# Optimization experiments

Measured on AMD Instinct MI355X. Metric: run time of the kernel, lower is better.

The kernel has to match this reference:

```python
import jax, jax.numpy as jnp
import numpy as np

B, S, D, H, DK = 2, 2048, 256, 8, 32


def setup_inputs() -> dict:
    key = jax.random.key(0)
    ks = jax.random.split(key, 12)
    inp = {
        "query": jax.random.normal(ks[0], (B, S, D), jnp.float32),
        "key_": jax.random.normal(ks[1], (B, S, D), jnp.float32),
        "value": jax.random.normal(ks[2], (B, S, D), jnp.float32),
        "mask": jax.random.randint(ks[3], (B, S, S), 0, 2).astype(bool),
        "relation": jax.random.normal(ks[4], (B, S, S), jnp.float32) * 0.05,
        # learned params (Linear stores y = x @ W^T; we store W already transposed)
        "Wq": jax.random.normal(ks[5], (D, H * DK), jnp.float32) * 0.02,
        "Wk": jax.random.normal(ks[6], (D, H * DK), jnp.float32) * 0.02,
        "Wv": jax.random.normal(ks[7], (D, H * DK), jnp.float32) * 0.02,
        "Wfc": jax.random.normal(ks[8], (H * DK, D), jnp.float32) * 0.02,
        "bfc": jax.random.normal(ks[9], (D,), jnp.float32) * 0.02,
        "gamma": jnp.ones((D,), jnp.float32),
        "beta": jnp.zeros((D,), jnp.float32),
    }
    return inp


def _layernorm(x, gamma, beta, eps=1e-5):
    mu = jnp.mean(x, axis=-1, keepdims=True)
    var = jnp.var(x, axis=-1, keepdims=True)
    return (x - mu) * jax.lax.rsqrt(var + eps) * gamma + beta


def reference(query, key_, value, mask, relation, Wq, Wk, Wv, Wfc, bfc, gamma, beta):
    b, s, _ = query.shape
    def split_heads(x, W):
        return (x @ W).reshape(b, s, H, DK).transpose(0, 2, 1, 3)  # [B,H,S,DK]
    Q = split_heads(query, Wq)
    K = split_heads(key_, Wk)
    V = split_heads(value, Wv)
    # (Q K^T) @ relation / sqrt(dk)   -- relation broadcast over heads
    qk = jnp.einsum('bhqd,bhkd->bhqk', Q, K)          # [B,H,S,S]
    scores = jnp.einsum('bhqk,bkn->bhqn', qk, relation) / jnp.sqrt(jnp.float32(DK))
    scores = jnp.where(mask[:, None, :, :], jnp.float32(-1e9), scores)
    attn = jax.nn.softmax(scores, axis=-1)            # dropout in eval mode = identity
    att = jnp.einsum('bhqn,bhnd->bhqd', attn, V)      # [B,H,S,DK]
    att = att.transpose(0, 2, 1, 3).reshape(b, s, H * DK)
    out = att @ Wfc + bfc
    return _layernorm(out + query, gamma, beta), attn
```

## Files before the change

kernel.cpp:

```cpp
#include <hip/hip_runtime.h>

constexpr int Bc = 2, Sc = 2048, Dc = 256, Hc = 8, DKc = 32;
constexpr int BH = Bc * Hc;

typedef _Float16 f16x8 __attribute__((ext_vector_type(8)));
typedef _Float16 f16x4 __attribute__((ext_vector_type(4)));
typedef float    f32x4 __attribute__((ext_vector_type(4)));

__global__ __launch_bounds__(256) void prep_kernel(
    const float* __restrict__ query, const float* __restrict__ key_,
    const float* __restrict__ value, const float* __restrict__ Wq,
    const float* __restrict__ Wk, const float* __restrict__ Wv,
    const float* __restrict__ rel, const unsigned int* __restrict__ mask,
    _Float16* __restrict__ Qb, _Float16* __restrict__ Kt,
    _Float16* __restrict__ Vt, _Float16* __restrict__ relT,
    unsigned int* __restrict__ mbits)
{
    __shared__ __align__(16) char smem[16640];
    const int bx = blockIdx.x;
    const int t = threadIdx.x;
    if (bx < 1536) {
        constexpr int ROWS = 8;
        float (*xs)[Dc] = (float(*)[Dc])smem;
        const int z = bx >> 9;
        const int lb = bx & 511;
        const float* X = (z == 0) ? query : (z == 1) ? key_ : value;
        const float* W = (z == 0) ? Wq : (z == 1) ? Wk : Wv;
        _Float16* out = (z == 0) ? Qb : (z == 1) ? Kt : Vt;
        const int vtrans = (z != 0);
        const float scale = (z == 0) ? 0.17677669529663689f : 1.0f;
        const int r0 = lb * ROWS;
        #pragma unroll
        for (int i = 0; i < ROWS; ++i)
            xs[i][t] = X[(long)(r0 + i) * Dc + t];
        __syncthreads();
        float acc[ROWS];
        #pragma unroll
        for (int i = 0; i < ROWS; ++i) acc[i] = 0.f;
        for (int d = 0; d < Dc; ++d) {
            float w = W[d * Dc + t];
            #pragma unroll
            for (int i = 0; i < ROWS; ++i) acc[i] = fmaf(xs[i][d], w, acc[i]);
        }
        const int h = t >> 5, dk = t & 31;
        #pragma unroll
        for (int i = 0; i < ROWS; ++i) {
            int row = r0 + i;
            int b = row >> 11, s = row & 2047;
            long idx = vtrans ? (((long)(b * Hc + h) * DKc + dk) * Sc + s)
                              : (((long)(b * Hc + h) * Sc + s) * DKc + dk);
            out[idx] = (_Float16)(acc[i] * scale);
        }
    } else if (bx < 3584) {
        float (*tile)[65] = (float(*)[65])smem;
        const int idx = bx - 1536;
        const int b = idx >> 10;
        const int rem = idx & 1023;
        const int k0 = (rem >> 5) * 64, n0 = (rem & 31) * 64;
        const int r = t >> 4;
        const int c4 = (t & 15) * 4;
        const float* src = rel + (long)b * Sc * Sc;
        #pragma unroll
        for (int i = 0; i < 4; ++i) {
            f32x4 v = *(const f32x4*)&src[(long)(k0 + i * 16 + r) * Sc + n0 + c4];
            *(f32x4*)&tile[i * 16 + r][c4] = v;
        }
        __syncthreads();
        _Float16* dst = relT + (long)b * Sc * Sc;
        #pragma unroll
        for (int i = 0; i < 4; ++i) {
            const int n = i * 16 + r;
            f16x4 o;
            #pragma unroll
            for (int e = 0; e < 4; ++e) o[e] = (_Float16)tile[c4 + e][n];
            *(f16x4*)&dst[(long)(n0 + n) * Sc + k0 + c4] = o;
        }
    } else {
        const int idx = (bx - 3584) * 256 + t;
        const uint4 a = ((const uint4*)mask)[idx * 2];
        const uint4 b = ((const uint4*)mask)[idx * 2 + 1];
        unsigned int wsv[8] = {a.x, a.y, a.z, a.w, b.x, b.y, b.z, b.w};
        unsigned int r = 0;
        #pragma unroll
        for (int j = 0; j < 8; ++j) {
            unsigned int nib = (wsv[j] | (wsv[j] >> 7) | (wsv[j] >> 14) | (wsv[j] >> 21)) & 0xFu;
            r |= nib << (4 * j);
        }
        mbits[idx] = r;
    }
}

__global__ __launch_bounds__(256) void kr_kernel(
    const _Float16* __restrict__ relT, const _Float16* __restrict__ Kt,
    float* __restrict__ KRp)
{
    constexpr int LDK = 72;
    __shared__ _Float16 As[64][LDK];
    __shared__ _Float16 Bs[64][LDK];
    const int z = blockIdx.z;
    const int b = z >> 1, ks = z & 1;
    const int m0 = blockIdx.y * 64;
    const int n0 = blockIdx.x * 64;
    const _Float16* Ap = relT + (long)b * Sc * Sc;
    const _Float16* Bp = Kt + (long)b * Hc * DKc * Sc;
    const int t = threadIdx.x;
    const int lane = t & 63, wave = t >> 6;
    const int wr = wave >> 1, wc = wave & 1;
    const int c = lane & 15, g = lane >> 4;
    const int lrow = t >> 2;
    const int lcol = (t & 3) * 16;
    f32x4 acc[2][2] = {};
    for (int k0 = ks * 1024; k0 < ks * 1024 + 1024; k0 += 64) {
        *(f16x8*)&As[lrow][lcol]     = *(const f16x8*)&Ap[(long)(m0 + lrow) * Sc + k0 + lcol];
        *(f16x8*)&As[lrow][lcol + 8] = *(const f16x8*)&Ap[(long)(m0 + lrow) * Sc + k0 + lcol + 8];
        *(f16x8*)&Bs[lrow][lcol]     = *(const f16x8*)&Bp[(long)(n0 + lrow) * Sc + k0 + lcol];
        *(f16x8*)&Bs[lrow][lcol + 8] = *(const f16x8*)&Bp[(long)(n0 + lrow) * Sc + k0 + lcol + 8];
        __syncthreads();
        #pragma unroll
        for (int kk = 0; kk < 2; ++kk) {
            const int kb = kk * 32 + g * 8;
            f16x8 af[2], bf[2];
            #pragma unroll
            for (int m = 0; m < 2; ++m)
                af[m] = *(const f16x8*)&As[wr * 32 + m * 16 + c][kb];
            #pragma unroll
            for (int n = 0; n < 2; ++n)
                bf[n] = *(const f16x8*)&Bs[wc * 32 + n * 16 + c][kb];
            #pragma unroll
            for (int m = 0; m < 2; ++m)
                #pragma unroll
                for (int n = 0; n < 2; ++n)
                    acc[m][n] = __builtin_amdgcn_mfma_f32_16x16x32_f16(
                        af[m], bf[n], acc[m][n], 0, 0, 0);
        }
        __syncthreads();
    }
    float* outp = KRp + ((long)ks * Bc + b) * Sc * 256;
    #pragma unroll
    for (int m = 0; m < 2; ++m)
        #pragma unroll
        for (int n = 0; n < 2; ++n)
            #pragma unroll
            for (int i = 0; i < 4; ++i) {
                int row = m0 + wr * 32 + m * 16 + g * 4 + i;
                int col = n0 + wc * 32 + n * 16 + c;
                outp[(long)row * 256 + col] = acc[m][n][i];
            }
}

__global__ __launch_bounds__(256) void krc_kernel(
    const float* __restrict__ KRp, _Float16* __restrict__ KRT)
{
    const long idx = ((long)blockIdx.x * 256 + threadIdx.x) * 4;
    const long half = (long)Bc * Sc * 256;
    f32x4 a = *(const f32x4*)&KRp[idx];
    f32x4 b = *(const f32x4*)&KRp[half + idx];
    f16x4 o;
    #pragma unroll
    for (int i = 0; i < 4; ++i) o[i] = (_Float16)(a[i] + b[i]);
    *(f16x4*)&KRT[idx] = o;
}

__global__ __launch_bounds__(256) void attn_pv_kernel(
    const _Float16* __restrict__ Qb,
    const _Float16* __restrict__ KRT,
    const _Float16* __restrict__ Vt,
    const unsigned int* __restrict__ mbits,
    float* __restrict__ esum_p,
    float* __restrict__ accp)
{
    constexpr int NT = 128, LDP = 136;
    __shared__ _Float16 p_lds[64][LDP];
    const int bh = blockIdx.y;
    const int ns = blockIdx.z;
    const int b = bh >> 3, h = bh & 7;
    const int q0 = blockIdx.x * 64;
    const int t = threadIdx.x, lane = t & 63, w = t >> 6;
    const int c = lane & 15, g = lane >> 4;
    const int q = q0 + w * 16 + c;
    const f16x8 qf = *(const f16x8*)&Qb[((long)bh * Sc + q) * DKc + g * 8];
    const _Float16* krt = KRT + (long)b * Sc * 256 + h * 32;
    const unsigned int* mbitrow = mbits + ((long)b * Sc + q) * (Sc / 32);
    const f32x4 zero = {};
    f32x4 acc[2] = {};
    float esum = 0.f;

    for (int nt = ns * 4; nt < ns * 4 + 4; ++nt) {
        const int n0 = nt * NT;
        f32x4 s[8];
        #pragma unroll
        for (int nf = 0; nf < 8; ++nf) {
            f16x8 kf = *(const f16x8*)&krt[(long)(n0 + nf * 16 + c) * 256 + g * 8];
            s[nf] = __builtin_amdgcn_mfma_f32_16x16x32_f16(kf, qf, zero, 0, 0, 0);
        }
        const uint4 mq = *(const uint4*)&mbitrow[nt * 4];
        const unsigned int mwv[4] = {mq.x, mq.y, mq.z, mq.w};
        #pragma unroll
        for (int nf = 0; nf < 8; ++nf) {
            const unsigned int bits = mwv[nf >> 1] >> ((nf & 1) * 16 + g * 4);
            f16x4 pv;
            #pragma unroll
            for (int i = 0; i < 4; ++i) {
                float p = ((bits >> i) & 1u) ? 0.f : __expf(s[nf][i]);
                esum += p;
                pv[i] = (_Float16)p;
            }
            *(f16x4*)&p_lds[w * 16 + c][nf * 16 + g * 4] = pv;
        }
        #pragma unroll
        for (int ks = 0; ks < 4; ++ks) {
            f16x8 af = *(const f16x8*)&p_lds[w * 16 + c][ks * 32 + g * 8];
            #pragma unroll
            for (int nb = 0; nb < 2; ++nb) {
                f16x8 vf = *(const f16x8*)&Vt[((long)bh * DKc + nb * 16 + c) * Sc + n0 + ks * 32 + g * 8];
                acc[nb] = __builtin_amdgcn_mfma_f32_16x16x32_f16(af, vf, acc[nb], 0, 0, 0);
            }
        }
    }
    esum += __shfl_xor(esum, 16);
    esum += __shfl_xor(esum, 32);
    if (lane < 16)
        esum_p[((long)ns * BH + bh) * Sc + q0 + w * 16 + lane] = esum;
    #pragma unroll
    for (int nb = 0; nb < 2; ++nb)
        #pragma unroll
        for (int i = 0; i < 4; ++i) {
            const long qrow = q0 + w * 16 + g * 4 + i;
            accp[(((long)ns * BH + bh) * Sc + qrow) * 32 + nb * 16 + c] = acc[nb][i];
        }
}

__global__ __launch_bounds__(256) void attn_store_kernel(
    const _Float16* __restrict__ Qb,
    const _Float16* __restrict__ KRT,
    const unsigned int* __restrict__ mbits,
    const float* __restrict__ esum_p,
    float* __restrict__ attn_out)
{
    constexpr int LDA = 132;
    __shared__ float a_lds[4][16][LDA];
    const int nt = blockIdx.x;
    const int q0 = blockIdx.y * 64;
    const int bh = blockIdx.z;
    const int b = bh >> 3, h = bh & 7;
    const int t = threadIdx.x, lane = t & 63, w = t >> 6;
    const int c = lane & 15, g = lane >> 4;
    const int q = q0 + w * 16 + c;
    const int n0 = nt * 128;
    const f16x8 qf = *(const f16x8*)&Qb[((long)bh * Sc + q) * DKc + g * 8];
    const _Float16* krt = KRT + (long)b * Sc * 256 + h * 32;
    const long row = (long)bh * Sc + q;
    const long BHS = (long)BH * Sc;
    const float es = esum_p[row] + esum_p[BHS + row]
                   + esum_p[2 * BHS + row] + esum_p[3 * BHS + row];
    const float rinv = 1.f / es;
    const f32x4 zero = {};

    f32x4 s[8];
    #pragma unroll
    for (int nf = 0; nf < 8; ++nf) {
        f16x8 kf = *(const f16x8*)&krt[(long)(n0 + nf * 16 + c) * 256 + g * 8];
        s[nf] = __builtin_amdgcn_mfma_f32_16x16x32_f16(kf, qf, zero, 0, 0, 0);
    }
    const uint4 mq = *(const uint4*)&mbits[((long)b * Sc + q) * (Sc / 32) + nt * 4];
    const unsigned int mwv[4] = {mq.x, mq.y, mq.z, mq.w};
    #pragma unroll
    for (int nf = 0; nf < 8; ++nf) {
        const unsigned int bits = mwv[nf >> 1] >> ((nf & 1) * 16 + g * 4);
        f32x4 av;
        #pragma unroll
        for (int i = 0; i < 4; ++i)
            av[i] = ((bits >> i) & 1u) ? 0.f : __expf(s[nf][i]) * rinv;
        *(f32x4*)&a_lds[w][c][nf * 16 + g * 4] = av;
    }
    float* aoutw = attn_out + (long)bh * Sc * Sc
                 + (long)(q0 + w * 16 + (lane >> 5)) * Sc + (lane & 31) * 4 + n0;
    #pragma unroll
    for (int r2 = 0; r2 < 8; ++r2) {
        f32x4 v = *(const f32x4*)&a_lds[w][r2 * 2 + (lane >> 5)][(lane & 31) * 4];
        __builtin_nontemporal_store(v, (f32x4*)&aoutw[(long)(r2 * 2) * Sc]);
    }
}

__global__ __launch_bounds__(256) void out_kernel(
    const float* __restrict__ accp,
    const float* __restrict__ esum_p,
    const float* __restrict__ Wfc,
    const float* __restrict__ bfc, const float* __restrict__ query,
    const float* __restrict__ gamma, const float* __restrict__ beta,
    float* __restrict__ out)
{
    __shared__ float xs[4][Dc];
    __shared__ float ys[4][Dc];
    const int r0 = blockIdx.x * 4;
    const int t = threadIdx.x;
    const int h = t >> 5, dk = t & 31;
    const long BHS = (long)BH * Sc;
    #pragma unroll
    for (int i = 0; i < 4; ++i) {
        const long row = r0 + i;
        const int b = (int)(row >> 11);
        const int q = (int)(row & 2047);
        const long bhq = ((long)(b * Hc + h)) * Sc + q;
        float es = 0.f, av = 0.f;
        #pragma unroll
        for (int ns = 0; ns < 4; ++ns) {
            es += esum_p[ns * BHS + bhq];
            av += accp[(ns * BHS + bhq) * 32 + dk];
        }
        xs[i][t] = av / es;
    }
    __syncthreads();
    float acc[4] = {0.f, 0.f, 0.f, 0.f};
    for (int d = 0; d < Dc; ++d) {
        float wv = Wfc[d * Dc + t];
        #pragma unroll
        for (int i = 0; i < 4; ++i) acc[i] = fmaf(xs[i][d], wv, acc[i]);
    }
    const float bias = bfc[t];
    #pragma unroll
    for (int i = 0; i < 4; ++i)
        ys[i][t] = acc[i] + bias + query[(long)(r0 + i) * Dc + t];
    __syncthreads();
    const int w = t >> 6, lane = t & 63;
    float x0 = ys[w][lane], x1 = ys[w][lane + 64];
    float x2 = ys[w][lane + 128], x3 = ys[w][lane + 192];
    float sum = x0 + x1 + x2 + x3;
    float sq = x0 * x0 + x1 * x1 + x2 * x2 + x3 * x3;
    for (int off = 32; off; off >>= 1) {
        sum += __shfl_down(sum, off);
        sq  += __shfl_down(sq, off);
    }
    sum = __shfl(sum, 0);
    sq  = __shfl(sq, 0);
    const float mu = sum * (1.f / 256.f);
    const float var = sq * (1.f / 256.f) - mu * mu;
    const float rstd = rsqrtf(var + 1e-5f);
    float* orow = out + (long)(r0 + w) * Dc;
    orow[lane]       = (x0 - mu) * rstd * gamma[lane]       + beta[lane];
    orow[lane + 64]  = (x1 - mu) * rstd * gamma[lane + 64]  + beta[lane + 64];
    orow[lane + 128] = (x2 - mu) * rstd * gamma[lane + 128] + beta[lane + 128];
    orow[lane + 192] = (x3 - mu) * rstd * gamma[lane + 192] + beta[lane + 192];
}

extern "C" void kernel_launch(void* const* d_in, const int* in_sizes, int n_in,
                              void* d_out, int out_size, void* d_ws, size_t ws_size,
                              hipStream_t stream)
{
    const float* query   = (const float*)d_in[0];
    const float* key_    = (const float*)d_in[1];
    const float* value   = (const float*)d_in[2];
    const unsigned int* mask = (const unsigned int*)d_in[3];
    const float* relation = (const float*)d_in[4];
    const float* Wq  = (const float*)d_in[5];
    const float* Wk  = (const float*)d_in[6];
    const float* Wv  = (const float*)d_in[7];
    const float* Wfc = (const float*)d_in[8];
    const float* bfc = (const float*)d_in[9];
    const float* gamma = (const float*)d_in[10];
    const float* beta  = (const float*)d_in[11];

    float* out_ln   = (float*)d_out;
    float* out_attn = (float*)d_out + (size_t)Bc * Sc * Dc;

    char* ws = (char*)d_ws;
    _Float16* Qb   = (_Float16*)(ws + 0);
    _Float16* Kt   = (_Float16*)(ws + 2097152);
    _Float16* Vt   = (_Float16*)(ws + 4194304);
    _Float16* relT = (_Float16*)(ws + 6291456);
    _Float16* KRT  = (_Float16*)(ws + 23068672);
    unsigned int* mbits = (unsigned int*)(ws + 29360128);
    float*    KRp   = (float*)  (ws + 30539776);
    float*    esum_p= (float*)  (ws + 38928384);
    float*    accp  = (float*)  (ws + 39452672);

    prep_kernel<<<dim3(4096), 256, 0, stream>>>(
        query, key_, value, Wq, Wk, Wv, relation, mask,
        Qb, Kt, Vt, relT, mbits);
    kr_kernel<<<dim3(4, Sc / 64, Bc * 2), 256, 0, stream>>>(relT, Kt, KRp);
    krc_kernel<<<dim3(Bc * Sc * 256 / 4 / 256), 256, 0, stream>>>(KRp, KRT);
    attn_pv_kernel<<<dim3(Sc / 64, BH, 4), 256, 0, stream>>>(
        Qb, KRT, Vt, mbits, esum_p, accp);
    attn_store_kernel<<<dim3(Sc / 128, Sc / 64, BH), 256, 0, stream>>>(
        Qb, KRT, mbits, esum_p, out_attn);
    out_kernel<<<dim3(Bc * Sc / 4), 256, 0, stream>>>(accp, esum_p, Wfc, bfc,
                                                      query, gamma, beta, out_ln);
}
```

Baseline: 196.9 us.

## Fuse relation transpose into KR GEMM and merge attn store with output kernel

```diff
diff --git a/kernel.cpp b/kernel.cpp
--- a/kernel.cpp
+++ b/kernel.cpp
@@ -11,17 +11,15 @@
     const float* __restrict__ query, const float* __restrict__ key_,
     const float* __restrict__ value, const float* __restrict__ Wq,
     const float* __restrict__ Wk, const float* __restrict__ Wv,
-    const float* __restrict__ rel, const unsigned int* __restrict__ mask,
+    const unsigned int* __restrict__ mask,
     _Float16* __restrict__ Qb, _Float16* __restrict__ Kt,
-    _Float16* __restrict__ Vt, _Float16* __restrict__ relT,
-    unsigned int* __restrict__ mbits)
-{
-    __shared__ __align__(16) char smem[16640];
+    _Float16* __restrict__ Vt, unsigned int* __restrict__ mbits)
+{
+    __shared__ float xs[8][Dc];
     const int bx = blockIdx.x;
     const int t = threadIdx.x;
     if (bx < 1536) {
         constexpr int ROWS = 8;
-        float (*xs)[Dc] = (float(*)[Dc])smem;
         const int z = bx >> 9;
         const int lb = bx & 511;
         const float* X = (z == 0) ? query : (z == 1) ? key_ : value;
@@ -51,32 +49,8 @@
                               : (((long)(b * Hc + h) * Sc + s) * DKc + dk);
             out[idx] = (_Float16)(acc[i] * scale);
         }
-    } else if (bx < 3584) {
-        float (*tile)[65] = (float(*)[65])smem;
-        const int idx = bx - 1536;
-        const int b = idx >> 10;
-        const int rem = idx & 1023;
-        const int k0 = (rem >> 5) * 64, n0 = (rem & 31) * 64;
-        const int r = t >> 4;
-        const int c4 = (t & 15) * 4;
-        const float* src = rel + (long)b * Sc * Sc;
-        #pragma unroll
-        for (int i = 0; i < 4; ++i) {
-            f32x4 v = *(const f32x4*)&src[(long)(k0 + i * 16 + r) * Sc + n0 + c4];
-            *(f32x4*)&tile[i * 16 + r][c4] = v;
-        }
-        __syncthreads();
-        _Float16* dst = relT + (long)b * Sc * Sc;
-        #pragma unroll
-        for (int i = 0; i < 4; ++i) {
-            const int n = i * 16 + r;
-            f16x4 o;
-            #pragma unroll
-            for (int e = 0; e < 4; ++e) o[e] = (_Float16)tile[c4 + e][n];
-            *(f16x4*)&dst[(long)(n0 + n) * Sc + k0 + c4] = o;
-        }
     } else {
-        const int idx = (bx - 3584) * 256 + t;
+        const int idx = (bx - 1536) * 256 + t;
         const uint4 a = ((const uint4*)mask)[idx * 2];
         const uint4 b = ((const uint4*)mask)[idx * 2 + 1];
         unsigned int wsv[8] = {a.x, a.y, a.z, a.w, b.x, b.y, b.z, b.w};
@@ -91,28 +65,31 @@
 }
 
 __global__ __launch_bounds__(256) void kr_kernel(
-    const _Float16* __restrict__ relT, const _Float16* __restrict__ Kt,
+    const float* __restrict__ rel, const _Float16* __restrict__ Kt,
     float* __restrict__ KRp)
 {
-    constexpr int LDK = 72;
-    __shared__ _Float16 As[64][LDK];
-    __shared__ _Float16 Bs[64][LDK];
+    __shared__ float tile[64][65];
+    __shared__ _Float16 Bs[64][72];
     const int z = blockIdx.z;
-    const int b = z >> 1, ks = z & 1;
+    const int b = z >> 2, ks = z & 3;
     const int m0 = blockIdx.y * 64;
     const int n0 = blockIdx.x * 64;
-    const _Float16* Ap = relT + (long)b * Sc * Sc;
+    const float* Ap = rel + (long)b * Sc * Sc;
     const _Float16* Bp = Kt + (long)b * Hc * DKc * Sc;
     const int t = threadIdx.x;
     const int lane = t & 63, wave = t >> 6;
     const int wr = wave >> 1, wc = wave & 1;
     const int c = lane & 15, g = lane >> 4;
+    const int rr = t >> 4;
+    const int c4 = (t & 15) * 4;
     const int lrow = t >> 2;
     const int lcol = (t & 3) * 16;
     f32x4 acc[2][2] = {};
-    for (int k0 = ks * 1024; k0 < ks * 1024 + 1024; k0 += 64) {
-        *(f16x8*)&As[lrow][lcol]     = *(const f16x8*)&Ap[(long)(m0 + lrow) * Sc + k0 + lcol];
-        *(f16x8*)&As[lrow][lcol + 8] = *(const f16x8*)&Ap[(long)(m0 + lrow) * Sc + k0 + lcol + 8];
+    for (int k0 = ks * 512; k0 < ks * 512 + 512; k0 += 64) {
+        #pragma unroll
+        for (int i = 0; i < 4; ++i)
+            *(f32x4*)&tile[i * 16 + rr][c4] =
+                *(const f32x4*)&Ap[(long)(k0 + i * 16 + rr) * Sc + m0 + c4];
         *(f16x8*)&Bs[lrow][lcol]     = *(const f16x8*)&Bp[(long)(n0 + lrow) * Sc + k0 + lcol];
         *(f16x8*)&Bs[lrow][lcol + 8] = *(const f16x8*)&Bp[(long)(n0 + lrow) * Sc + k0 + lcol + 8];
         __syncthreads();
@@ -121,8 +98,12 @@
             const int kb = kk * 32 + g * 8;
             f16x8 af[2], bf[2];
             #pragma unroll
-            for (int m = 0; m < 2; ++m)
-                af[m] = *(const f16x8*)&As[wr * 32 + m * 16 + c][kb];
+            for (int m = 0; m < 2; ++m) {
+                const int nrow = wr * 32 + m * 16 + c;
+                #pragma unroll
+                for (int j = 0; j < 8; ++j)
+                    af[m][j] = (_Float16)tile[kb + j][nrow];
+            }
             #pragma unroll
             for (int n = 0; n < 2; ++n)
                 bf[n] = *(const f16x8*)&Bs[wc * 32 + n * 16 + c][kb];
@@ -152,12 +133,17 @@
     const float* __restrict__ KRp, _Float16* __restrict__ KRT)
 {
     const long idx = ((long)blockIdx.x * 256 + threadIdx.x) * 4;
-    const long half = (long)Bc * Sc * 256;
-    f32x4 a = *(const f32x4*)&KRp[idx];
-    f32x4 b = *(const f32x4*)&KRp[half + idx];
+    const long P = (long)Bc * Sc * 256;
+    f32x4 s = {};
+    #pragma unroll
+    for (int p = 0; p < 4; ++p) {
+        f32x4 v = *(const f32x4*)&KRp[p * P + idx];
+        #pragma unroll
+        for (int i = 0; i < 4; ++i) s[i] += v[i];
+    }
     f16x4 o;
     #pragma unroll
-    for (int i = 0; i < 4; ++i) o[i] = (_Float16)(a[i] + b[i]);
+    for (int i = 0; i < 4; ++i) o[i] = (_Float16)s[i];
     *(f16x4*)&KRT[idx] = o;
 }
 
@@ -230,117 +216,123 @@
         }
 }
 
-__global__ __launch_bounds__(256) void attn_store_kernel(
+__global__ __launch_bounds__(256) void finish_kernel(
     const _Float16* __restrict__ Qb,
     const _Float16* __restrict__ KRT,
     const unsigned int* __restrict__ mbits,
     const float* __restrict__ esum_p,
-    float* __restrict__ attn_out)
-{
-    constexpr int LDA = 132;
-    __shared__ float a_lds[4][16][LDA];
-    const int nt = blockIdx.x;
-    const int q0 = blockIdx.y * 64;
-    const int bh = blockIdx.z;
-    const int b = bh >> 3, h = bh & 7;
-    const int t = threadIdx.x, lane = t & 63, w = t >> 6;
-    const int c = lane & 15, g = lane >> 4;
-    const int q = q0 + w * 16 + c;
-    const int n0 = nt * 128;
-    const f16x8 qf = *(const f16x8*)&Qb[((long)bh * Sc + q) * DKc + g * 8];
-    const _Float16* krt = KRT + (long)b * Sc * 256 + h * 32;
-    const long row = (long)bh * Sc + q;
+    const float* __restrict__ accp,
+    const float* __restrict__ Wfc, const float* __restrict__ bfc,
+    const float* __restrict__ query, const float* __restrict__ gamma,
+    const float* __restrict__ beta,
+    float* __restrict__ attn_out,
+    float* __restrict__ out_ln)
+{
+    __shared__ __align__(16) char smem[33792];
+    const int z = blockIdx.z;
+    const int t = threadIdx.x;
     const long BHS = (long)BH * Sc;
-    const float es = esum_p[row] + esum_p[BHS + row]
-                   + esum_p[2 * BHS + row] + esum_p[3 * BHS + row];
-    const float rinv = 1.f / es;
-    const f32x4 zero = {};
-
-    f32x4 s[8];
-    #pragma unroll
-    for (int nf = 0; nf < 8; ++nf) {
-        f16x8 kf = *(const f16x8*)&krt[(long)(n0 + nf * 16 + c) * 256 + g * 8];
-        s[nf] = __builtin_amdgcn_mfma_f32_16x16x32_f16(kf, qf, zero, 0, 0, 0);
-    }
-    const uint4 mq = *(const uint4*)&mbits[((long)b * Sc + q) * (Sc / 32) + nt * 4];
-    const unsigned int mwv[4] = {mq.x, mq.y, mq.z, mq.w};
-    #pragma unroll
-    for (int nf = 0; nf < 8; ++nf) {
-        const unsigned int bits = mwv[nf >> 1] >> ((nf & 1) * 16 + g * 4);
-        f32x4 av;
-        #pragma unroll
-        for (int i = 0; i < 4; ++i)
-            av[i] = ((bits >> i) & 1u) ? 0.f : __expf(s[nf][i]) * rinv;
-        *(f32x4*)&a_lds[w][c][nf * 16 + g * 4] = av;
-    }
-    float* aoutw = attn_out + (long)bh * Sc * Sc
-                 + (long)(q0 + w * 16 + (lane >> 5)) * Sc + (lane & 31) * 4 + n0;
-    #pragma unroll
-    for (int r2 = 0; r2 < 8; ++r2) {
-        f32x4 v = *(const f32x4*)&a_lds[w][r2 * 2 + (lane >> 5)][(lane & 31) * 4];
-        __builtin_nontemporal_store(v, (f32x4*)&aoutw[(long)(r2 * 2) * Sc]);
-    }
-}
-
-__global__ __launch_bounds__(256) void out_kernel(
-    const float* __restrict__ accp,
-    const float* __restrict__ esum_p,
-    const float* __restrict__ Wfc,
-    const float* __restrict__ bfc, const float* __restrict__ query,
-    const float* __restrict__ gamma, const float* __restrict__ beta,
-    float* __restrict__ out)
-{
-    __shared__ float xs[4][Dc];
-    __shared__ float ys[4][Dc];
-    const int r0 = blockIdx.x * 4;
-    const int t = threadIdx.x;
-    const int h = t >> 5, dk = t & 31;
-    const long BHS = (long)BH * Sc;
-    #pragma unroll
-    for (int i = 0; i < 4; ++i) {
-        const long row = r0 + i;
-        const int b = (int)(row >> 11);
-        const int q = (int)(row & 2047);
-        const long bhq = ((long)(b * Hc + h)) * Sc + q;
-        float es = 0.f, av = 0.f;
-        #pragma unroll
-        for (int ns = 0; ns < 4; ++ns) {
-            es += esum_p[ns * BHS + bhq];
-            av += accp[(ns * BHS + bhq) * 32 + dk];
-        }
-        xs[i][t] = av / es;
-    }
-    __syncthreads();
-    float acc[4] = {0.f, 0.f, 0.f, 0.f};
-    for (int d = 0; d < Dc; ++d) {
-        float wv = Wfc[d * Dc + t];
-        #pragma unroll
-        for (int i = 0; i < 4; ++i) acc[i] = fmaf(xs[i][d], wv, acc[i]);
-    }
-    const float bias = bfc[t];
-    #pragma unroll
-    for (int i = 0; i < 4; ++i)
-        ys[i][t] = acc[i] + bias + query[(long)(r0 + i) * Dc + t];
-    __syncthreads();
-    const int w = t >> 6, lane = t & 63;
-    float x0 = ys[w][lane], x1 = ys[w][lane + 64];
-    float x2 = ys[w][lane + 128], x3 = ys[w][lane + 192];
-    float sum = x0 + x1 + x2 + x3;
-    float sq = x0 * x0 + x1 * x1 + x2 * x2 + x3 * x3;
-    for (int off = 32; off; off >>= 1) {
-        sum += __shfl_down(sum, off);
-        sq  += __shfl_down(sq, off);
-    }
-    sum = __shfl(sum, 0);
-    sq  = __shfl(sq, 0);
-    const float mu = sum * (1.f / 256.f);
-    const float var = sq * (1.f / 256.f) - mu * mu;
-    const float rstd = rsqrtf(var + 1e-5f);
-    float* orow = out + (long)(r0 + w) * Dc;
-    orow[lane]       = (x0 - mu) * rstd * gamma[lane]       + beta[lane];
-    orow[lane + 64]  = (x1 - mu) * rstd * gamma[lane + 64]  + beta[lane + 64];
-    orow[lane + 128] = (x2 - mu) * rstd * gamma[lane + 128] + beta[lane + 128];
-    orow[lane + 192] = (x3 - mu) * rstd * gamma[lane + 192] + beta[lane + 192];
+    if (z < 16) {
+        constexpr int LDA = 132;
+        float (*a_lds)[16][LDA] = (float(*)[16][LDA])smem;
+        const int nt = blockIdx.x;
+        const int q0 = blockIdx.y * 64;
+        const int bh = z;
+        const int b = bh >> 3, h = bh & 7;
+        const int lane = t & 63, w = t >> 6;
+        const int c = lane & 15, g = lane >> 4;
+        const int q = q0 + w * 16 + c;
+        const int n0 = nt * 128;
+        const f16x8 qf = *(const f16x8*)&Qb[((long)bh * Sc + q) * DKc + g * 8];
+        const _Float16* krt = KRT + (long)b * Sc * 256 + h * 32;
+        const long row = (long)bh * Sc + q;
+        const float es = esum_p[row] + esum_p[BHS + row]
+                       + esum_p[2 * BHS + row] + esum_p[3 * BHS + row];
+        const float rinv = 1.f / es;
+        const f32x4 zero = {};
+
+        f32x4 s[8];
+        #pragma unroll
+        for (int nf = 0; nf < 8; ++nf) {
+            f16x8 kf = *(const f16x8*)&krt[(long)(n0 + nf * 16 + c) * 256 + g * 8];
+            s[nf] = __builtin_amdgcn_mfma_f32_16x16x32_f16(kf, qf, zero, 0, 0, 0);
+        }
+        const uint4 mq = *(const uint4*)&mbits[((long)b * Sc + q) * (Sc / 32) + nt * 4];
+        const unsigned int mwv[4] = {mq.x, mq.y, mq.z, mq.w};
+        #pragma unroll
+        for (int nf = 0; nf < 8; ++nf) {
+            const unsigned int bits = mwv[nf >> 1] >> ((nf & 1) * 16 + g * 4);
+            f32x4 av;
+            #pragma unroll
+            for (int i = 0; i < 4; ++i)
+                av[i] = ((bits >> i) & 1u) ? 0.f : __expf(s[nf][i]) * rinv;
+            *(f32x4*)&a_lds[w][c][nf * 16 + g * 4] = av;
+        }
+        float* aoutw = attn_out + (long)bh * Sc * Sc
+                     + (long)(q0 + w * 16 + (lane >> 5)) * Sc + (lane & 31) * 4 + n0;
+        #pragma unroll
+        for (int r2 = 0; r2 < 8; ++r2) {
+            f32x4 v = *(const f32x4*)&a_lds[w][r2 * 2 + (lane >> 5)][(lane & 31) * 4];
+            __builtin_nontemporal_store(v, (f32x4*)&aoutw[(long)(r2 * 2) * Sc]);
+        }
+    } else {
+        float (*xs)[Dc] = (float(*)[Dc])smem;
+        float (*ys)[Dc] = (float(*)[Dc])(smem + 8 * Dc * 4);
+        const int flat = blockIdx.x * 32 + blockIdx.y;
+        const int r0 = flat * 8;
+        const int h = t >> 5, dk = t & 31;
+        #pragma unroll
+        for (int i = 0; i < 8; ++i) {
+            const long row = r0 + i;
+            const int b = (int)(row >> 11);
+            const int q = (int)(row & 2047);
+            const long bhq = ((long)(b * Hc + h)) * Sc + q;
+            float es = 0.f, av = 0.f;
+            #pragma unroll
+            for (int ns = 0; ns < 4; ++ns) {
+                es += esum_p[ns * BHS + bhq];
+                av += accp[(ns * BHS + bhq) * 32 + dk];
+            }
+            xs[i][t] = av / es;
+        }
+        __syncthreads();
+        float acc[8];
+        #pragma unroll
+        for (int i = 0; i < 8; ++i) acc[i] = 0.f;
+        for (int d = 0; d < Dc; ++d) {
+            float wv = Wfc[d * Dc + t];
+            #pragma unroll
+            for (int i = 0; i < 8; ++i) acc[i] = fmaf(xs[i][d], wv, acc[i]);
+        }
+        const float bias = bfc[t];
+        #pragma unroll
+        for (int i = 0; i < 8; ++i)
+            ys[i][t] = acc[i] + bias + query[(long)(r0 + i) * Dc + t];
+        __syncthreads();
+        const int w = t >> 6, lane = t & 63;
+        #pragma unroll
+        for (int rr2 = 0; rr2 < 2; ++rr2) {
+            const int ri = w * 2 + rr2;
+            float x0 = ys[ri][lane], x1 = ys[ri][lane + 64];
+            float x2 = ys[ri][lane + 128], x3 = ys[ri][lane + 192];
+            float sum = x0 + x1 + x2 + x3;
+            float sq = x0 * x0 + x1 * x1 + x2 * x2 + x3 * x3;
+            for (int off = 32; off; off >>= 1) {
+                sum += __shfl_down(sum, off);
+                sq  += __shfl_down(sq, off);
+            }
+            sum = __shfl(sum, 0);
+            sq  = __shfl(sq, 0);
+            const float mu = sum * (1.f / 256.f);
+            const float var = sq * (1.f / 256.f) - mu * mu;
+            const float rstd = rsqrtf(var + 1e-5f);
+            float* orow = out_ln + (long)(r0 + ri) * Dc;
+            orow[lane]       = (x0 - mu) * rstd * gamma[lane]       + beta[lane];
+            orow[lane + 64]  = (x1 - mu) * rstd * gamma[lane + 64]  + beta[lane + 64];
+            orow[lane + 128] = (x2 - mu) * rstd * gamma[lane + 128] + beta[lane + 128];
+            orow[lane + 192] = (x3 - mu) * rstd * gamma[lane + 192] + beta[lane + 192];
+        }
+    }
 }
 
 extern "C" void kernel_launch(void* const* d_in, const int* in_sizes, int n_in,
@@ -367,22 +359,19 @@
     _Float16* Qb   = (_Float16*)(ws + 0);
     _Float16* Kt   = (_Float16*)(ws + 2097152);
     _Float16* Vt   = (_Float16*)(ws + 4194304);
-    _Float16* relT = (_Float16*)(ws + 6291456);
-    _Float16* KRT  = (_Float16*)(ws + 23068672);
-    unsigned int* mbits = (unsigned int*)(ws + 29360128);
-    float*    KRp   = (float*)  (ws + 30539776);
-    float*    esum_p= (float*)  (ws + 38928384);
-    float*    accp  = (float*)  (ws + 39452672);
-
-    prep_kernel<<<dim3(4096), 256, 0, stream>>>(
-        query, key_, value, Wq, Wk, Wv, relation, mask,
-        Qb, Kt, Vt, relT, mbits);
-    kr_kernel<<<dim3(4, Sc / 64, Bc * 2), 256, 0, stream>>>(relT, Kt, KRp);
-    krc_kernel<<<dim3(Bc * Sc * 256 / 4 / 256), 256, 0, stream>>>(KRp, KRT);
+    _Float16* KRT  = (_Float16*)(ws + 6291456);
+    unsigned int* mbits = (unsigned int*)(ws + 8388608);
+    float*    KRp   = (float*)  (ws + 9437184);
+    float*    esum_p= (float*)  (ws + 26214400);
+    float*    accp  = (float*)  (ws + 26738688);
+
+    prep_kernel<<<dim3(2560), 256, 0, stream>>>(
+        query, key_, value, Wq, Wk, Wv, mask, Qb, Kt, Vt, mbits);
+    kr_kernel<<<dim3(4, Sc / 64, Bc * 4), 256, 0, stream>>>(relation, Kt, KRp);
+    krc_kernel<<<dim3(1024), 256, 0, stream>>>(KRp, KRT);
     attn_pv_kernel<<<dim3(Sc / 64, BH, 4), 256, 0, stream>>>(
         Qb, KRT, Vt, mbits, esum_p, accp);
-    attn_store_kernel<<<dim3(Sc / 128, Sc / 64, BH), 256, 0, stream>>>(
-        Qb, KRT, mbits, esum_p, out_attn);
-    out_kernel<<<dim3(Bc * Sc / 4), 256, 0, stream>>>(accp, esum_p, Wfc, bfc,
-                                                      query, gamma, beta, out_ln);
-}
+    finish_kernel<<<dim3(Sc / 128, Sc / 64, 17), 256, 0, stream>>>(
+        Qb, KRT, mbits, esum_p, accp, Wfc, bfc, query, gamma, beta,
+        out_attn, out_ln);
+}
```

Result: slower. 214.1 us (+8.7%).
